# Kernel optimization log

Measured on AMD Instinct MI355X. Metric: run time of the kernel, lower is better.

The kernel has to match this reference:

```python
import jax, jax.numpy as jnp
import numpy as np

N = 32768          # B*T flattened tokens
E = 1024           # embed_dim
H = 16             # num_heads
D = E // H         # head_dim = 64


def setup_inputs() -> dict:
    key = jax.random.key(0)
    ks = jax.random.split(key, 9)
    w = lambda k: jax.random.normal(k, (E, E), jnp.float32) * (E ** -0.5)
    b = lambda k: jax.random.normal(k, (E,), jnp.float32) * 0.01
    return {
        "x": jax.random.normal(ks[0], (N, E), jnp.float32),
        "Wq": w(ks[1]), "bq": b(ks[2]),
        "Wk": w(ks[3]), "bk": b(ks[4]),
        "Wv": w(ks[5]), "bv": b(ks[6]),
        "Wo": w(ks[7]), "bo": b(ks[8]),
    }


def reference(x, Wq, bq, Wk, bk, Wv, bv, Wo, bo):
    # nn.Linear: y = x @ W^T + b
    q = (x @ Wq.T + bq).reshape(-1, H, D)   # [N, H, D]
    k = (x @ Wk.T + bk).reshape(-1, H, D)
    v = (x @ Wv.T + bv).reshape(-1, H, D)
    scale = D ** -0.5
    # per-token attention ACROSS HEADS: scores [N, H, H]
    qk = jnp.einsum('nhd,nHd->nhH', q, k) * scale
    attn = jax.nn.softmax(qk, axis=-1)      # softmax over key-heads
    out = jnp.einsum('nhH,nHd->nhd', attn, v).reshape(-1, E)
    return out @ Wo.T + bo                  # [N, E]
```

## Files before the change

### kernel.cpp

```cpp
#include <hip/hip_runtime.h>

typedef __attribute__((ext_vector_type(8))) short short8;
typedef __attribute__((ext_vector_type(8))) unsigned short ushort8;
typedef __attribute__((ext_vector_type(4))) float f32x4;

__device__ __forceinline__ float b2f(short s) {
    unsigned u = ((unsigned)(unsigned short)s) << 16;
    return __builtin_bit_cast(float, u);
}
__device__ __forceinline__ unsigned short f2b(float f) {
    unsigned u = __builtin_bit_cast(unsigned, f);
    u += 0x7fffu + ((u >> 16) & 1u);
    return (unsigned short)(u >> 16);
}

__device__ __forceinline__ void gload_lds16(const void* gptr, void* ldsptr) {
    typedef __attribute__((address_space(1))) const void gv_t;
    typedef __attribute__((address_space(3))) void lv_t;
    gv_t* g = reinterpret_cast<gv_t*>(reinterpret_cast<unsigned long long>(gptr));
    lv_t* l = reinterpret_cast<lv_t*>((unsigned int)reinterpret_cast<unsigned long long>(ldsptr));
    __builtin_amdgcn_global_load_lds(g, l, 16, 0, 0);
}

#define MEMFENCE() asm volatile("" ::: "memory")
#define BARRIER() do { MEMFENCE(); __builtin_amdgcn_s_barrier(); MEMFENCE(); } while (0)

__global__ __launch_bounds__(256) void cvt_bf16(const float* __restrict__ in,
                                                unsigned short* __restrict__ out,
                                                int n8) {
    int i = blockIdx.x * 256 + threadIdx.x;
    if (i >= n8) return;
    const float4* p = (const float4*)in + (size_t)i * 2;
    float4 a = p[0], b = p[1];
    ushort8 o;
    o[0] = f2b(a.x); o[1] = f2b(a.y); o[2] = f2b(a.z); o[3] = f2b(a.w);
    o[4] = f2b(b.x); o[5] = f2b(b.y); o[6] = f2b(b.z); o[7] = f2b(b.w);
    *(ushort8*)(out + (size_t)i * 8) = o;
}

__global__ __launch_bounds__(256) void concat3(const float* __restrict__ a,
                                               const float* __restrict__ b,
                                               const float* __restrict__ c,
                                               float* __restrict__ o) {
    int i = blockIdx.x * 256 + threadIdx.x;
    float v = (i < 1024) ? a[i] : (i < 2048 ? b[i - 1024] : c[i - 2048]);
    o[i] = v;
}

template <bool OUT_BF16>
__global__ __launch_bounds__(512, 2) void gemm_bt(const short* __restrict__ A,
                                                  const short* __restrict__ B,
                                                  const float* __restrict__ bias,
                                                  unsigned short* __restrict__ Cb,
                                                  float* __restrict__ Cf,
                                                  int M, int N, int K) {
    extern __shared__ short lds[];
    short* Ab = lds;
    short* Bb = lds + 2 * 2 * 128 * 64;

    const int lane = threadIdx.x & 63;
    const int wave = threadIdx.x >> 6;
    const int wr = wave >> 2;
    const int wc = wave & 3;

    const int nwg = gridDim.x;
    const int bid = blockIdx.x;
    const int swz = (bid & 7) * (nwg >> 3) + (bid >> 3);
    const int ncol = N >> 8;
    const int trow = swz / ncol, tcol = swz % ncol;

    const short* Ablk = A + (size_t)trow * 256 * K;
    const short* Bblk = B + (size_t)tcol * 256 * K;

    const int scol_sw = ((lane & 7) ^ (lane >> 3)) * 8;
    const int rl = lane & 15;
    const int g0 = (((lane >> 4)) ^ (lane & 7)) * 8;
    const int g1 = ((4 + (lane >> 4)) ^ (lane & 7)) * 8;

    short8 af[4][2];
    short8 bf[4][2];
    f32x4 acc[8][4] = {};

    const int NT = K >> 6;
    const int smax = 4 * (NT - 2);

    auto stage_half = [&](int ts, int h) {
        const int dd = ts & 1;
        const int hh = h & 1;
        const short* gb = ((h < 2) ? Ablk : Bblk) + (size_t)(hh * 128) * K + (ts << 6) + scol_sw;
        short* lb = ((h < 2) ? Ab : Bb) + (((dd << 1) | hh) << 13);
#pragma unroll
        for (int c = 0; c < 2; ++c) {
            const int row = c * 64 + wave * 8 + (lane >> 3);
            gload_lds16(gb + (size_t)row * K, lb + ((c * 64 + wave * 8) << 6));
        }
    };
    auto stage_if = [&](int s) { if (s >= 0 && s < smax) stage_half((s >> 2) + 2, s & 3); };

    auto readA = [&](int d, int mh) {
        const short* base = Ab + (((d << 1) | wr) << 13) + ((mh * 64 + rl) << 6);
#pragma unroll
        for (int m = 0; m < 4; ++m) {
            af[m][0] = *(const short8*)(base + ((m * 16) << 6) + g0);
            af[m][1] = *(const short8*)(base + ((m * 16) << 6) + g1);
        }
    };
    auto readB = [&](int d, int nh) {
        const short* base = Bb + (((d << 1) | (wc >> 1)) << 13) + (((wc & 1) * 64 + rl) << 6);
#pragma unroll
        for (int j = 0; j < 2; ++j) {
            bf[nh * 2 + j][0] = *(const short8*)(base + (((nh * 2 + j) * 16) << 6) + g0);
            bf[nh * 2 + j][1] = *(const short8*)(base + (((nh * 2 + j) * 16) << 6) + g1);
        }
    };
    auto mm = [&](int mh, int nh) {
        __builtin_amdgcn_s_setprio(1);
#pragma unroll
        for (int ks = 0; ks < 2; ++ks)
#pragma unroll
            for (int m = 0; m < 4; ++m)
#pragma unroll
                for (int j = 0; j < 2; ++j)
                    acc[mh * 4 + m][nh * 2 + j] = __builtin_amdgcn_mfma_f32_16x16x32_bf16(
                        af[m][ks], bf[nh * 2 + j][ks], acc[mh * 4 + m][nh * 2 + j], 0, 0, 0);
        __builtin_amdgcn_s_setprio(0);
    };

    auto tile_body = [&](int T, int d) {
        const int s0 = 4 * T;
        readA(d, 0); readB(d, 0);
        stage_if(s0 - 3);
        asm volatile("s_waitcnt lgkmcnt(8)" ::: "memory");
        BARRIER();
        asm volatile("s_waitcnt lgkmcnt(0)" ::: "memory");
        mm(0, 0);
        BARRIER();
        readB(d, 1);
        stage_if(s0 - 2);
        BARRIER();
        asm volatile("s_waitcnt lgkmcnt(0)" ::: "memory");
        mm(0, 1);
        BARRIER();
        readA(d, 1);
        stage_if(s0 - 1);
        BARRIER();
        asm volatile("s_waitcnt lgkmcnt(0)" ::: "memory");
        mm(1, 0);
        BARRIER();
        stage_if(s0);
        BARRIER();
        mm(1, 1);
        if (T < NT - 2)       asm volatile("s_waitcnt vmcnt(2)" ::: "memory");
        else if (T == NT - 2) asm volatile("s_waitcnt vmcnt(0)" ::: "memory");
        BARRIER();
    };

#pragma unroll
    for (int t = 0; t < 2; ++t)
#pragma unroll
        for (int h = 0; h < 4; ++h) stage_half(t, h);
    asm volatile("s_waitcnt vmcnt(8)" ::: "memory");
    BARRIER();

    for (int T2 = 0; T2 < NT; T2 += 2) {
        tile_body(T2, 0);
        tile_body(T2 + 1, 1);
    }

    const int crow0 = trow * 256 + wr * 128 + (lane >> 4) * 4;
    const int ccol0 = tcol * 256 + wc * 64 + rl;
#pragma unroll
    for (int n = 0; n < 4; ++n) {
        const int col = ccol0 + n * 16;
        const float bv = bias[col];
#pragma unroll
        for (int m = 0; m < 8; ++m) {
            const int row0 = crow0 + m * 16;
#pragma unroll
            for (int r = 0; r < 4; ++r) {
                float val = acc[m][n][r] + bv;
                if (OUT_BF16) Cb[(size_t)(row0 + r) * N + col] = f2b(val);
                else          Cf[(size_t)(row0 + r) * N + col] = val;
            }
        }
    }
}

__global__ __launch_bounds__(256) void attn_k(const short* __restrict__ qkv,
                                              short* __restrict__ out) {
    int gid = blockIdx.x * 256 + threadIdx.x;
    int t = gid >> 4, h = gid & 15;
    const short* q  = qkv + (size_t)t * 3072 + h * 64;
    const short* kb = qkv + (size_t)t * 3072 + 1024;
    const short* vb = qkv + (size_t)t * 3072 + 2048;

    float qf[64];
#pragma unroll
    for (int j = 0; j < 8; ++j) {
        short8 qv = *(const short8*)(q + j * 8);
#pragma unroll
        for (int i = 0; i < 8; ++i) qf[j * 8 + i] = b2f(qv[i]);
    }

    float s[16];
    float mx = -1e30f;
#pragma unroll
    for (int g = 0; g < 16; ++g) {
        float a = 0.f;
#pragma unroll
        for (int j = 0; j < 8; ++j) {
            short8 kv = *(const short8*)(kb + g * 64 + j * 8);
#pragma unroll
            for (int i = 0; i < 8; ++i) a += qf[j * 8 + i] * b2f(kv[i]);
        }
        s[g] = a * 0.125f;
        mx = fmaxf(mx, s[g]);
    }
    float den = 0.f;
#pragma unroll
    for (int g = 0; g < 16; ++g) { s[g] = __expf(s[g] - mx); den += s[g]; }
    float inv = 1.f / den;

#pragma unroll
    for (int j = 0; j < 8; ++j) {
        float o[8] = {0.f, 0.f, 0.f, 0.f, 0.f, 0.f, 0.f, 0.f};
#pragma unroll
        for (int g = 0; g < 16; ++g) {
            short8 vv = *(const short8*)(vb + g * 64 + j * 8);
            float w = s[g];
#pragma unroll
            for (int i = 0; i < 8; ++i) o[i] += w * b2f(vv[i]);
        }
        short8 ov;
#pragma unroll
        for (int i = 0; i < 8; ++i) ov[i] = (short)f2b(o[i] * inv);
        *(short8*)(out + (size_t)t * 1024 + h * 64 + j * 8) = ov;
    }
}

extern "C" void kernel_launch(void* const* d_in, const int* in_sizes, int n_in,
                              void* d_out, int out_size, void* d_ws, size_t ws_size,
                              hipStream_t stream) {
    const float* x  = (const float*)d_in[0];
    const float* Wq = (const float*)d_in[1];
    const float* bq = (const float*)d_in[2];
    const float* Wk = (const float*)d_in[3];
    const float* bk = (const float*)d_in[4];
    const float* Wv = (const float*)d_in[5];
    const float* bv = (const float*)d_in[6];
    const float* Wo = (const float*)d_in[7];
    const float* bo = (const float*)d_in[8];
    float* out = (float*)d_out;

    const int N = 32768, E = 1024;
    const int LDS_BYTES = 131072;

    (void)hipFuncSetAttribute((const void*)gemm_bt<true>,  hipFuncAttributeMaxDynamicSharedMemorySize, LDS_BYTES);
    (void)hipFuncSetAttribute((const void*)gemm_bt<false>, hipFuncAttributeMaxDynamicSharedMemorySize, LDS_BYTES);

    char* ws = (char*)d_ws;
    size_t off = 0;
    short* xb = (short*)(ws + off);         off += (size_t)N * E * 2;
    short* wqkv = (short*)(ws + off);       off += (size_t)3 * E * E * 2;
    short* wo = (short*)(ws + off);         off += (size_t)E * E * 2;
    float* bqkv = (float*)(ws + off);       off += (size_t)3 * E * 4;
    off = (off + 255) & ~(size_t)255;
    short* y1 = (short*)(ws + off);         off += (size_t)N * 3 * E * 2;
    short* ao = xb;

    cvt_bf16<<<dim3((N * E / 8 + 255) / 256), dim3(256), 0, stream>>>(x, (unsigned short*)xb, N * E / 8);
    cvt_bf16<<<dim3((E * E / 8 + 255) / 256), dim3(256), 0, stream>>>(Wq, (unsigned short*)wqkv, E * E / 8);
    cvt_bf16<<<dim3((E * E / 8 + 255) / 256), dim3(256), 0, stream>>>(Wk, (unsigned short*)(wqkv + (size_t)E * E), E * E / 8);
    cvt_bf16<<<dim3((E * E / 8 + 255) / 256), dim3(256), 0, stream>>>(Wv, (unsigned short*)(wqkv + (size_t)2 * E * E), E * E / 8);
    cvt_bf16<<<dim3((E * E / 8 + 255) / 256), dim3(256), 0, stream>>>(Wo, (unsigned short*)wo, E * E / 8);
    concat3<<<dim3(12), dim3(256), 0, stream>>>(bq, bk, bv, bqkv);

    gemm_bt<true><<<dim3((N / 256) * (3 * E / 256)), dim3(512), LDS_BYTES, stream>>>(
        xb, wqkv, bqkv, (unsigned short*)y1, nullptr, N, 3 * E, E);

    attn_k<<<dim3(N * 16 / 256), dim3(256), 0, stream>>>(y1, ao);

    gemm_bt<false><<<dim3((N / 256) * (E / 256)), dim3(512), LDS_BYTES, stream>>>(
        ao, wo, bo, nullptr, out, N, E, E);
}
```

Measured before the change: 478.0 us.

## Merge conversion kernels and add prefetch-pipelined GEMM for output projection

Folds the five bf16 conversion launches and the bias concat into one kernel to cut launch overhead. Adds a new output-projection GEMM with K-step 32, a double-buffered 64KB LDS layout, and staged global-to-LDS loads interleaved with MFMA quarter-blocks under explicit waitcnt and setprio control. The aim is to overlap memory traffic with matrix math and allow higher occupancy. The hand-tuned waitcnt counts are fragile and could stall or race if they are miscounted.

```diff
diff --git a/kernel.cpp b/kernel.cpp
--- a/kernel.cpp
+++ b/kernel.cpp
@@ -25,26 +25,44 @@
 #define MEMFENCE() asm volatile("" ::: "memory")
 #define BARRIER() do { MEMFENCE(); __builtin_amdgcn_s_barrier(); MEMFENCE(); } while (0)
 
-__global__ __launch_bounds__(256) void cvt_bf16(const float* __restrict__ in,
-                                                unsigned short* __restrict__ out,
-                                                int n8) {
-    int i = blockIdx.x * 256 + threadIdx.x;
-    if (i >= n8) return;
-    const float4* p = (const float4*)in + (size_t)i * 2;
+__global__ __launch_bounds__(256) void cvt_all(const float* __restrict__ x,
+                                               const float* __restrict__ Wq,
+                                               const float* __restrict__ Wk,
+                                               const float* __restrict__ Wv,
+                                               const float* __restrict__ Wo,
+                                               const float* __restrict__ bq,
+                                               const float* __restrict__ bk,
+                                               const float* __restrict__ bv,
+                                               unsigned short* __restrict__ xb,
+                                               unsigned short* __restrict__ wqkv,
+                                               unsigned short* __restrict__ wo,
+                                               float* __restrict__ bqkv) {
+    const int bid = blockIdx.x;
+    const float* src;
+    unsigned short* dst;
+    int base8;
+    if (bid < 16384)      { src = x;  dst = xb;              base8 = bid; }
+    else if (bid < 16896) { src = Wq; dst = wqkv;            base8 = bid - 16384; }
+    else if (bid < 17408) { src = Wk; dst = wqkv + 1048576;  base8 = bid - 16896; }
+    else if (bid < 17920) { src = Wv; dst = wqkv + 2097152;  base8 = bid - 17408; }
+    else if (bid < 18432) { src = Wo; dst = wo;              base8 = bid - 17920; }
+    else {
+        const int i = threadIdx.x;
+#pragma unroll
+        for (int r = 0; r < 12; ++r) {
+            int j = r * 256 + i;
+            float v = (j < 1024) ? bq[j] : (j < 2048 ? bk[j - 1024] : bv[j - 2048]);
+            bqkv[j] = v;
+        }
+        return;
+    }
+    const size_t i8 = (size_t)base8 * 256 + threadIdx.x;
+    const float4* p = (const float4*)src + i8 * 2;
     float4 a = p[0], b = p[1];
     ushort8 o;
     o[0] = f2b(a.x); o[1] = f2b(a.y); o[2] = f2b(a.z); o[3] = f2b(a.w);
     o[4] = f2b(b.x); o[5] = f2b(b.y); o[6] = f2b(b.z); o[7] = f2b(b.w);
-    *(ushort8*)(out + (size_t)i * 8) = o;
-}
-
-__global__ __launch_bounds__(256) void concat3(const float* __restrict__ a,
-                                               const float* __restrict__ b,
-                                               const float* __restrict__ c,
-                                               float* __restrict__ o) {
-    int i = blockIdx.x * 256 + threadIdx.x;
-    float v = (i < 1024) ? a[i] : (i < 2048 ? b[i - 1024] : c[i - 2048]);
-    o[i] = v;
+    *(ushort8*)(dst + i8 * 8) = o;
 }
 
 template <bool OUT_BF16>
@@ -182,6 +200,128 @@
                 if (OUT_BF16) Cb[(size_t)(row0 + r) * N + col] = f2b(val);
                 else          Cf[(size_t)(row0 + r) * N + col] = val;
             }
+        }
+    }
+}
+
+#define MMQ(AF, BF, MB, NB)                                                            \
+    do {                                                                               \
+        __builtin_amdgcn_s_setprio(1);                                                 \
+        _Pragma("unroll")                                                              \
+        for (int m_ = 0; m_ < 4; ++m_)                                                 \
+            _Pragma("unroll")                                                          \
+            for (int n_ = 0; n_ < 2; ++n_)                                             \
+                acc[(MB) + m_][(NB) + n_] = __builtin_amdgcn_mfma_f32_16x16x32_bf16(   \
+                    AF[m_], BF[n_], acc[(MB) + m_][(NB) + n_], 0, 0, 0);               \
+        __builtin_amdgcn_s_setprio(0);                                                 \
+    } while (0)
+
+__global__ __launch_bounds__(512, 2) void gemm_pf(const short* __restrict__ A,
+                                                  const short* __restrict__ B,
+                                                  const float* __restrict__ bias,
+                                                  float* __restrict__ Cf,
+                                                  int M, int N, int K) {
+    extern __shared__ short lds[];
+    const int lane = threadIdx.x & 63;
+    const int wave = threadIdx.x >> 6;
+    const int wr = wave >> 2;
+    const int wc = wave & 3;
+
+    const int nwg = gridDim.x;
+    const int bid = blockIdx.x;
+    const int swz = (bid & 7) * (nwg >> 3) + (bid >> 3);
+    const int ncol = N >> 8;
+    const int trow = swz / ncol, tcol = swz % ncol;
+
+    const short* Ablk = A + (size_t)trow * 256 * K;
+    const short* Bblk = B + (size_t)tcol * 256 * K;
+
+    const int s_r = lane >> 2;
+    const int s_c = ((lane & 3) ^ ((lane >> 3) & 3)) * 8;
+    const int rl = lane & 15;
+    const int gph = ((lane >> 4) ^ ((rl >> 1) & 3)) * 8;
+
+    short8 af0[4], af1[4], bf0[2], bf1[2];
+    f32x4 acc[8][4] = {};
+
+    const int NT = K >> 5;
+    const int smax = 4 * (NT - 2);
+
+    auto stage_half = [&](int ts, int h) {
+        const int dd = ts & 1;
+        const int hh = h & 1;
+        const int R0 = hh * 128 + wave * 16;
+        const short* gb = (h < 2) ? Ablk : Bblk;
+        short* lb = lds + ((h < 2) ? 0 : 16384) + dd * 8192;
+        gload_lds16(gb + (size_t)(R0 + s_r) * K + (ts << 5) + s_c, lb + R0 * 32);
+    };
+    auto stage_if = [&](int s) { if (s >= 0 && s < smax) stage_half((s >> 2) + 2, s & 3); };
+
+    auto readA0 = [&](int d) {
+        const short* base = lds + d * 8192 + (wr * 128 + rl) * 32 + gph;
+#pragma unroll
+        for (int m = 0; m < 4; ++m) af0[m] = *(const short8*)(base + m * 16 * 32);
+    };
+    auto readA1 = [&](int d) {
+        const short* base = lds + d * 8192 + (wr * 128 + 64 + rl) * 32 + gph;
+#pragma unroll
+        for (int m = 0; m < 4; ++m) af1[m] = *(const short8*)(base + m * 16 * 32);
+    };
+    auto readB0 = [&](int d) {
+        const short* base = lds + 16384 + d * 8192 + (wc * 64 + rl) * 32 + gph;
+#pragma unroll
+        for (int j = 0; j < 2; ++j) bf0[j] = *(const short8*)(base + j * 16 * 32);
+    };
+    auto readB1 = [&](int d) {
+        const short* base = lds + 16384 + d * 8192 + (wc * 64 + 32 + rl) * 32 + gph;
+#pragma unroll
+        for (int j = 0; j < 2; ++j) bf1[j] = *(const short8*)(base + j * 16 * 32);
+    };
+
+#pragma unroll
+    for (int t = 0; t < 2; ++t)
+#pragma unroll
+        for (int h = 0; h < 4; ++h) stage_half(t, h);
+    asm volatile("s_waitcnt vmcnt(4)" ::: "memory");
+    BARRIER();
+    readA0(0); readB0(0);
+
+    for (int t = 0; t < NT; ++t) {
+        const int d = t & 1;
+        const int s0 = 4 * t;
+        stage_if(s0 - 3);
+        readA1(d);
+        asm volatile("s_waitcnt lgkmcnt(4)" ::: "memory");
+        MMQ(af0, bf0, 0, 0);
+        stage_if(s0 - 2);
+        readB1(d);
+        asm volatile("s_waitcnt lgkmcnt(2)" ::: "memory");
+        MMQ(af1, bf0, 4, 0);
+        BARRIER();
+        stage_if(s0 - 1);
+        asm volatile("s_waitcnt lgkmcnt(0)" ::: "memory");
+        MMQ(af0, bf1, 0, 2);
+        stage_if(s0);
+        if (t < NT - 2) asm volatile("s_waitcnt vmcnt(1)" ::: "memory");
+        else            asm volatile("s_waitcnt vmcnt(0)" ::: "memory");
+        BARRIER();
+        if (t + 1 < NT) { readA0(d ^ 1); readB0(d ^ 1); }
+        asm volatile("s_waitcnt lgkmcnt(6)" ::: "memory");
+        MMQ(af1, bf1, 4, 2);
+    }
+
+    const int crow0 = trow * 256 + wr * 128 + (lane >> 4) * 4;
+    const int ccol0 = tcol * 256 + wc * 64 + rl;
+#pragma unroll
+    for (int n = 0; n < 4; ++n) {
+        const int col = ccol0 + n * 16;
+        const float bv = bias[col];
+#pragma unroll
+        for (int m = 0; m < 8; ++m) {
+            const int row0 = crow0 + m * 16;
+#pragma unroll
+            for (int r = 0; r < 4; ++r)
+                Cf[(size_t)(row0 + r) * N + col] = acc[m][n][r] + bv;
         }
     }
 }
@@ -253,10 +393,9 @@
     float* out = (float*)d_out;
 
     const int N = 32768, E = 1024;
-    const int LDS_BYTES = 131072;
-
-    (void)hipFuncSetAttribute((const void*)gemm_bt<true>,  hipFuncAttributeMaxDynamicSharedMemorySize, LDS_BYTES);
-    (void)hipFuncSetAttribute((const void*)gemm_bt<false>, hipFuncAttributeMaxDynamicSharedMemorySize, LDS_BYTES);
+
+    (void)hipFuncSetAttribute((const void*)gemm_bt<true>, hipFuncAttributeMaxDynamicSharedMemorySize, 131072);
+    (void)hipFuncSetAttribute((const void*)gemm_pf,       hipFuncAttributeMaxDynamicSharedMemorySize, 65536);
 
     char* ws = (char*)d_ws;
     size_t off = 0;
@@ -268,18 +407,15 @@
     short* y1 = (short*)(ws + off);         off += (size_t)N * 3 * E * 2;
     short* ao = xb;
 
-    cvt_bf16<<<dim3((N * E / 8 + 255) / 256), dim3(256), 0, stream>>>(x, (unsigned short*)xb, N * E / 8);
-    cvt_bf16<<<dim3((E * E / 8 + 255) / 256), dim3(256), 0, stream>>>(Wq, (unsigned short*)wqkv, E * E / 8);
-    cvt_bf16<<<dim3((E * E / 8 + 255) / 256), dim3(256), 0, stream>>>(Wk, (unsigned short*)(wqkv + (size_t)E * E), E * E / 8);
-    cvt_bf16<<<dim3((E * E / 8 + 255) / 256), dim3(256), 0, stream>>>(Wv, (unsigned short*)(wqkv + (size_t)2 * E * E), E * E / 8);
-    cvt_bf16<<<dim3((E * E / 8 + 255) / 256), dim3(256), 0, stream>>>(Wo, (unsigned short*)wo, E * E / 8);
-    concat3<<<dim3(12), dim3(256), 0, stream>>>(bq, bk, bv, bqkv);
-
-    gemm_bt<true><<<dim3((N / 256) * (3 * E / 256)), dim3(512), LDS_BYTES, stream>>>(
+    cvt_all<<<dim3(18433), dim3(256), 0, stream>>>(
+        x, Wq, Wk, Wv, Wo, bq, bk, bv,
+        (unsigned short*)xb, (unsigned short*)wqkv, (unsigned short*)wo, bqkv);
+
+    gemm_bt<true><<<dim3((N / 256) * (3 * E / 256)), dim3(512), 131072, stream>>>(
         xb, wqkv, bqkv, (unsigned short*)y1, nullptr, N, 3 * E, E);
 
     attn_k<<<dim3(N * 16 / 256), dim3(256), 0, stream>>>(y1, ao);
 
-    gemm_bt<false><<<dim3((N / 256) * (E / 256)), dim3(512), LDS_BYTES, stream>>>(
-        ao, wo, bo, nullptr, out, N, E, E);
-}
+    gemm_pf<<<dim3((N / 256) * (E / 256)), dim3(512), 65536, stream>>>(
+        ao, wo, bo, out, N, E, E);
+}
```

Result: no change. 478.7 us (+0.1%).

## Merge conversion launches and stage per-token K/V in LDS for attention

Applied to the files above, without the earlier changes.

Six conversion and bias-concat launches are folded into one kernel that picks its source and destination by block index. This removes launch overhead. The attention kernel now has each block cooperatively load the K and V rows of 16 tokens into shared memory with coalesced 16-byte loads. Each thread then reads K/V from LDS, using a per-token rotation so the 16 threads of a token hit different banks, instead of every thread re-reading the same K/V rows from global memory. The cost is 64 KB of LDS per block, which may limit occupancy.

```diff
diff --git a/kernel.cpp b/kernel.cpp
--- a/kernel.cpp
+++ b/kernel.cpp
@@ -25,26 +25,44 @@
 #define MEMFENCE() asm volatile("" ::: "memory")
 #define BARRIER() do { MEMFENCE(); __builtin_amdgcn_s_barrier(); MEMFENCE(); } while (0)
 
-__global__ __launch_bounds__(256) void cvt_bf16(const float* __restrict__ in,
-                                                unsigned short* __restrict__ out,
-                                                int n8) {
-    int i = blockIdx.x * 256 + threadIdx.x;
-    if (i >= n8) return;
-    const float4* p = (const float4*)in + (size_t)i * 2;
+__global__ __launch_bounds__(256) void cvt_all(const float* __restrict__ x,
+                                               const float* __restrict__ Wq,
+                                               const float* __restrict__ Wk,
+                                               const float* __restrict__ Wv,
+                                               const float* __restrict__ Wo,
+                                               const float* __restrict__ bq,
+                                               const float* __restrict__ bk,
+                                               const float* __restrict__ bv,
+                                               unsigned short* __restrict__ xb,
+                                               unsigned short* __restrict__ wqkv,
+                                               unsigned short* __restrict__ wo,
+                                               float* __restrict__ bqkv) {
+    const int bid = blockIdx.x;
+    const float* src;
+    unsigned short* dst;
+    int base8;
+    if (bid < 16384)      { src = x;  dst = xb;              base8 = bid; }
+    else if (bid < 16896) { src = Wq; dst = wqkv;            base8 = bid - 16384; }
+    else if (bid < 17408) { src = Wk; dst = wqkv + 1048576;  base8 = bid - 16896; }
+    else if (bid < 17920) { src = Wv; dst = wqkv + 2097152;  base8 = bid - 17408; }
+    else if (bid < 18432) { src = Wo; dst = wo;              base8 = bid - 17920; }
+    else {
+        const int i = threadIdx.x;
+#pragma unroll
+        for (int r = 0; r < 12; ++r) {
+            int j = r * 256 + i;
+            float v = (j < 1024) ? bq[j] : (j < 2048 ? bk[j - 1024] : bv[j - 2048]);
+            bqkv[j] = v;
+        }
+        return;
+    }
+    const size_t i8 = (size_t)base8 * 256 + threadIdx.x;
+    const float4* p = (const float4*)src + i8 * 2;
     float4 a = p[0], b = p[1];
     ushort8 o;
     o[0] = f2b(a.x); o[1] = f2b(a.y); o[2] = f2b(a.z); o[3] = f2b(a.w);
     o[4] = f2b(b.x); o[5] = f2b(b.y); o[6] = f2b(b.z); o[7] = f2b(b.w);
-    *(ushort8*)(out + (size_t)i * 8) = o;
-}
-
-__global__ __launch_bounds__(256) void concat3(const float* __restrict__ a,
-                                               const float* __restrict__ b,
-                                               const float* __restrict__ c,
-                                               float* __restrict__ o) {
-    int i = blockIdx.x * 256 + threadIdx.x;
-    float v = (i < 1024) ? a[i] : (i < 2048 ? b[i - 1024] : c[i - 2048]);
-    o[i] = v;
+    *(ushort8*)(dst + i8 * 8) = o;
 }
 
 template <bool OUT_BF16>
@@ -186,13 +204,23 @@
     }
 }
 
-__global__ __launch_bounds__(256) void attn_k(const short* __restrict__ qkv,
-                                              short* __restrict__ out) {
-    int gid = blockIdx.x * 256 + threadIdx.x;
-    int t = gid >> 4, h = gid & 15;
-    const short* q  = qkv + (size_t)t * 3072 + h * 64;
-    const short* kb = qkv + (size_t)t * 3072 + 1024;
-    const short* vb = qkv + (size_t)t * 3072 + 2048;
+__global__ __launch_bounds__(256) void attn2(const short* __restrict__ qkv,
+                                             short* __restrict__ out) {
+    __shared__ short kv[16 * 2048];
+    const int tid = threadIdx.x;
+    const size_t t0 = (size_t)blockIdx.x * 16;
+
+#pragma unroll
+    for (int r = 0; r < 16; ++r) {
+        short8 v = *(const short8*)(qkv + (t0 + r) * 3072 + 1024 + tid * 8);
+        *(short8*)(kv + r * 2048 + ((tid * 8 + r * 8) & 2047)) = v;
+    }
+    __syncthreads();
+
+    const int t = tid >> 4, h = tid & 15;
+    const int rot = t * 8;
+    const short* kt = kv + t * 2048;
+    const short* q = qkv + (t0 + t) * 3072 + h * 64;
 
     float qf[64];
 #pragma unroll
@@ -209,9 +237,9 @@
         float a = 0.f;
 #pragma unroll
         for (int j = 0; j < 8; ++j) {
-            short8 kv = *(const short8*)(kb + g * 64 + j * 8);
-#pragma unroll
-            for (int i = 0; i < 8; ++i) a += qf[j * 8 + i] * b2f(kv[i]);
+            short8 kvv = *(const short8*)(kt + ((g * 64 + j * 8 + rot) & 2047));
+#pragma unroll
+            for (int i = 0; i < 8; ++i) a += qf[j * 8 + i] * b2f(kvv[i]);
         }
         s[g] = a * 0.125f;
         mx = fmaxf(mx, s[g]);
@@ -226,7 +254,7 @@
         float o[8] = {0.f, 0.f, 0.f, 0.f, 0.f, 0.f, 0.f, 0.f};
 #pragma unroll
         for (int g = 0; g < 16; ++g) {
-            short8 vv = *(const short8*)(vb + g * 64 + j * 8);
+            short8 vv = *(const short8*)(kt + ((1024 + g * 64 + j * 8 + rot) & 2047));
             float w = s[g];
 #pragma unroll
             for (int i = 0; i < 8; ++i) o[i] += w * b2f(vv[i]);
@@ -234,7 +262,7 @@
         short8 ov;
 #pragma unroll
         for (int i = 0; i < 8; ++i) ov[i] = (short)f2b(o[i] * inv);
-        *(short8*)(out + (size_t)t * 1024 + h * 64 + j * 8) = ov;
+        *(short8*)(out + (t0 + t) * 1024 + h * 64 + j * 8) = ov;
     }
 }
 
@@ -268,17 +296,14 @@
     short* y1 = (short*)(ws + off);         off += (size_t)N * 3 * E * 2;
     short* ao = xb;
 
-    cvt_bf16<<<dim3((N * E / 8 + 255) / 256), dim3(256), 0, stream>>>(x, (unsigned short*)xb, N * E / 8);
-    cvt_bf16<<<dim3((E * E / 8 + 255) / 256), dim3(256), 0, stream>>>(Wq, (unsigned short*)wqkv, E * E / 8);
-    cvt_bf16<<<dim3((E * E / 8 + 255) / 256), dim3(256), 0, stream>>>(Wk, (unsigned short*)(wqkv + (size_t)E * E), E * E / 8);
-    cvt_bf16<<<dim3((E * E / 8 + 255) / 256), dim3(256), 0, stream>>>(Wv, (unsigned short*)(wqkv + (size_t)2 * E * E), E * E / 8);
-    cvt_bf16<<<dim3((E * E / 8 + 255) / 256), dim3(256), 0, stream>>>(Wo, (unsigned short*)wo, E * E / 8);
-    concat3<<<dim3(12), dim3(256), 0, stream>>>(bq, bk, bv, bqkv);
+    cvt_all<<<dim3(18433), dim3(256), 0, stream>>>(
+        x, Wq, Wk, Wv, Wo, bq, bk, bv,
+        (unsigned short*)xb, (unsigned short*)wqkv, (unsigned short*)wo, bqkv);
 
     gemm_bt<true><<<dim3((N / 256) * (3 * E / 256)), dim3(512), LDS_BYTES, stream>>>(
         xb, wqkv, bqkv, (unsigned short*)y1, nullptr, N, 3 * E, E);
 
-    attn_k<<<dim3(N * 16 / 256), dim3(256), 0, stream>>>(y1, ao);
+    attn2<<<dim3(N / 16), dim3(256), 0, stream>>>(y1, ao);
 
     gemm_bt<false><<<dim3((N / 256) * (E / 256)), dim3(512), LDS_BYTES, stream>>>(
         ao, wo, bo, nullptr, out, N, E, E);
```

Result: faster. 435.2 us (-9.0%).
